# Kernel tuning notes

Hardware: AMD Instinct MI355X
Metric: run time of the kernel (lower is better)

Reference implementation:

```python
import jax, jax.numpy as jnp
import numpy as np

N, K, D, M, P, HG, HD = 120000, 8, 64, 100000, 16, 32, 96
VOXEL, TAU, OCC_INC, LMIN, LMAX = 0.1, 0.3, 0.5, -2.0, 3.5


def setup_inputs() -> dict:
    ks = jax.random.split(jax.random.key(0), 20)
    f32 = jnp.float32
    s = 0.05
    return {
        'pts_xyz': jax.random.uniform(ks[0], (N, 3), f32) * 10.0,
        'f_pts': jax.random.normal(ks[1], (N, D), f32),
        'z_latent': jax.random.normal(ks[2], (M, D), f32),
        'vals_st': jax.random.normal(ks[3], (M,), f32) * 0.5,
        'centers_xyz': jax.random.uniform(ks[4], (M, 3), f32) * 10.0,
        'Wf': jax.random.normal(ks[5], (P, D), f32) * s,
        'Wz': jax.random.normal(ks[6], (P, D), f32) * s,
        'w_delta': jax.random.normal(ks[7], (1, 3), f32) * s,
        'b_delta': jnp.zeros((1,), f32),
        'log_temp': jnp.zeros((1,), f32),
        'W_ih': jax.random.normal(ks[8], (3 * D, D), f32) * s,
        'W_hh': jax.random.normal(ks[9], (3 * D, D), f32) * s,
        'b_ih': jnp.zeros((3 * D,), f32),
        'b_hh': jnp.zeros((3 * D,), f32),
        'Wg1': jax.random.normal(ks[10], (HG, 2 * D), f32) * s,
        'bg1': jnp.zeros((HG,), f32),
        'Wg2': jax.random.normal(ks[11], (1, HG), f32) * s,
        'bg2': jnp.zeros((1,), f32),
        'ln_g': jnp.ones((D,), f32),
        'ln_b': jnp.zeros((D,), f32),
        'Wd1': jax.random.normal(ks[12], (HD, D), f32) * s,
        'bd1': jnp.zeros((HD,), f32),
        'Wd2': jax.random.normal(ks[13], (HD, HD), f32) * s,
        'bd2': jnp.zeros((HD,), f32),
        'Wd3': jax.random.normal(ks[14], (1, HD), f32) * s,
        'bd3': jnp.zeros((1,), f32),
        'keys': jnp.sort(jax.random.randint(ks[15], (M,), 0, 2 ** 30, jnp.int32)),
        'cand_idx': jax.random.randint(ks[16], (N, K), 0, M, jnp.int32),
    }


def _forward(pts_xyz, f_pts, z_latent, vals_st, centers_xyz, Wf, Wz, w_delta, b_delta,
             log_temp, W_ih, W_hh, b_ih, b_hh, Wg1, bg1, Wg2, bg2, ln_g, ln_b,
             Wd1, bd1, Wd2, bd2, Wd3, bd3, keys, cand_idx):
    # --- sparse voxel hash lookup + log-odds scatter update ---
    ijk = jnp.floor(pts_xyz / VOXEL).astype(jnp.int32)
    off = jnp.int32(1 << 9)
    h = ((ijk[:, 0] + off) << 20) ^ ((ijk[:, 1] + off) << 10) ^ (ijk[:, 2] + off)
    vox_idx = jnp.clip(jnp.searchsorted(keys, h), 0, M - 1)  # (N,)
    vals_new = jnp.clip(vals_st.at[vox_idx].add(OCC_INC), LMIN, LMAX)

    # --- top-K low-temperature routing: sim(f, z, delta) ---
    z_c = z_latent[cand_idx]                                  # (N,K,D) gather
    delta = pts_xyz[:, None, :] - centers_xyz[cand_idx]       # (N,K,3)
    Fp = f_pts @ Wf.T                                         # (N,P)
    Zp = z_c @ Wz.T                                           # (N,K,P)
    Fp = Fp / (jnp.linalg.norm(Fp, axis=-1, keepdims=True) + 1e-6)
    Zp = Zp / (jnp.linalg.norm(Zp, axis=-1, keepdims=True) + 1e-6)
    core = jnp.einsum('np,nkp->nk', Fp, Zp)
    dterm = jnp.einsum('nkc,c->nk', delta, w_delta[0]) + b_delta[0]
    sim = jnp.exp(log_temp[0]) * (core + dterm)
    w = jax.nn.softmax(sim / TAU, axis=-1)                    # (N,K)

    # --- scatter weighted point features to voxels ---
    flat_idx = cand_idx.reshape(-1)                           # (N*K,)
    contrib = (w[..., None] * f_pts[:, None, :]).reshape(-1, D)
    msg = jax.ops.segment_sum(contrib, flat_idx, num_segments=M)   # (M,D)
    wsum = jax.ops.segment_sum(w.reshape(-1), flat_idx, num_segments=M)
    msg = msg / (wsum[:, None] + 1e-6)

    # --- per-voxel gate + GRU latent fusion ---
    gate_in = jnp.concatenate([z_latent, msg], axis=-1)       # (M,2D)
    g = jax.nn.sigmoid(jax.nn.relu(gate_in @ Wg1.T + bg1) @ Wg2.T + bg2)  # (M,1)
    gi = msg @ W_ih.T + b_ih
    gh = z_latent @ W_hh.T + b_hh
    gir, giz, gin = jnp.split(gi, 3, axis=-1)
    ghr, ghz, ghn = jnp.split(gh, 3, axis=-1)
    r = jax.nn.sigmoid(gir + ghr)
    u = jax.nn.sigmoid(giz + ghz)
    n = jnp.tanh(gin + r * ghn)
    h_new = (1.0 - u) * n + u * z_latent
    z_new = z_latent + g * (h_new - z_latent)                 # (M,D)

    # --- decode occupancy: LN -> fc1 -> residual fc2 -> fc3 -> sigmoid ---
    mu = z_new.mean(-1, keepdims=True)
    var = z_new.var(-1, keepdims=True)
    x = (z_new - mu) * jax.lax.rsqrt(var + 1e-5) * ln_g + ln_b
    hd = jax.nn.relu(x @ Wd1.T + bd1)
    hd = hd + jax.nn.relu(hd @ Wd2.T + bd2)
    p = jax.nn.sigmoid((hd @ Wd3.T + bd3)[:, 0])              # (M,)

    return jnp.concatenate([p, vals_new])                     # (2M,)


def reference(pts_xyz, f_pts, z_latent, vals_st, centers_xyz, Wf, Wz, w_delta, b_delta,
              log_temp, W_ih, W_hh, b_ih, b_hh, Wg1, bg1, Wg2, bg2, ln_g, ln_b,
              Wd1, bd1, Wd2, bd2, Wd3, bd3, keys, cand_idx):
    return _forward(pts_xyz, f_pts, z_latent, vals_st, centers_xyz, Wf, Wz, w_delta,
                    b_delta, log_temp, W_ih, W_hh, b_ih, b_hh, Wg1, bg1, Wg2, bg2,
                    ln_g, ln_b, Wd1, bd1, Wd2, bd2, Wd3, bd3, keys, cand_idx)
```

## Files before the change

kernel.cpp:

```cpp
#include <hip/hip_runtime.h>
#include <math.h>

#define Nn 120000
#define Kk 8
#define Dd 64
#define Mm 100000
#define Pp 16
#define HGg 32
#define HDd 96
#define CAP 40
#define LUTB 12

typedef __attribute__((ext_vector_type(8))) short bf16x8;
typedef __attribute__((ext_vector_type(4))) float f32x4;
typedef __attribute__((ext_vector_type(4))) float fx4;
typedef __attribute__((ext_vector_type(4))) int ix4;

#define PB_K0    1563
#define PB_PACK  (PB_K0 + 22)
#define PB_INIT  (PB_PACK + 391)

__device__ __forceinline__ float sigmoidf_(float x) { return 1.f / (1.f + __expf(-x)); }
__device__ __forceinline__ float tanh_fast(float x) {
    float e = __expf(2.f * x);
    return 1.f - 2.f / (e + 1.f);
}
__device__ __forceinline__ short f2bf(float f) {
    unsigned u = __float_as_uint(f);
    unsigned r = (u + 0x7fffu + ((u >> 16) & 1u)) >> 16;
    return (short)r;
}

__global__ __launch_bounds__(256) void k_prep_all(const float* __restrict__ z,
                                                  const float* __restrict__ Wz,
                                                  const float* __restrict__ centers,
                                                  const float* __restrict__ w_delta,
                                                  const int* __restrict__ keys,
                                                  const float* __restrict__ Wg1,
                                                  const float* __restrict__ W_ih,
                                                  const float* __restrict__ W_hh,
                                                  const float* __restrict__ Wd1,
                                                  const float* __restrict__ Wd2,
                                                  const float* __restrict__ vals,
                                                  unsigned* __restrict__ Zbf,
                                                  float* __restrict__ cdot,
                                                  int* __restrict__ lut,
                                                  short* __restrict__ wsW,
                                                  int* __restrict__ cnt,
                                                  float* __restrict__ vacc) {
    int b = blockIdx.x;
    if (b < PB_K0) {
        int g = threadIdx.x & 3;
        int m = b * 64 + (threadIdx.x >> 2);
        if (m >= Mm) return;
        if (g == 0 && m <= (1 << LUTB)) {
            int target = m << (30 - LUTB);
            int lo = 0, hi = Mm;
            while (lo < hi) {
                int mid = (lo + hi) >> 1;
                if (keys[mid] < target) lo = mid + 1; else hi = mid;
            }
            lut[m] = lo;
        }
        const float4* zr = (const float4*)(z + (size_t)m * Dd + g * 16);
        float4 q0 = zr[0], q1 = zr[1], q2 = zr[2], q3 = zr[3];
        float acc[Pp];
#pragma unroll
        for (int p = 0; p < Pp; p++) {
            const float4* w = (const float4*)(Wz + (size_t)p * Dd + g * 16);
            float4 w0 = w[0], w1 = w[1], w2 = w[2], w3 = w[3];
            float s = q0.x * w0.x + q0.y * w0.y + q0.z * w0.z + q0.w * w0.w;
            s += q1.x * w1.x + q1.y * w1.y + q1.z * w1.z + q1.w * w1.w;
            s += q2.x * w2.x + q2.y * w2.y + q2.z * w2.z + q2.w * w2.w;
            s += q3.x * w3.x + q3.y * w3.y + q3.z * w3.z + q3.w * w3.w;
            acc[p] = s;
        }
#pragma unroll
        for (int p = 0; p < Pp; p++) {
            acc[p] += __shfl_xor(acc[p], 1, 64);
            acc[p] += __shfl_xor(acc[p], 2, 64);
        }
        float ss = 0.f;
#pragma unroll
        for (int p = 0; p < Pp; p++) ss = fmaf(acc[p], acc[p], ss);
        float inv = 1.f / (sqrtf(ss) + 1e-6f);
        unsigned* row = Zbf + (size_t)m * 8;
        if (g < 2) {
            uint4 o;
            unsigned w[4];
#pragma unroll
            for (int j = 0; j < 4; j++) {
                float v0 = acc[g * 8 + 2 * j] * inv;
                float v1 = acc[g * 8 + 2 * j + 1] * inv;
                w[j] = (unsigned)(unsigned short)f2bf(v0)
                     | ((unsigned)(unsigned short)f2bf(v1) << 16);
            }
            o.x = w[0]; o.y = w[1]; o.z = w[2]; o.w = w[3];
            ((uint4*)row)[g] = o;
        } else if (g == 2) {
            cdot[m] = centers[3 * m] * w_delta[0] + centers[3 * m + 1] * w_delta[1]
                    + centers[3 * m + 2] * w_delta[2];
        }
    } else if (b < PB_PACK) {
        int idx = (b - PB_K0) * 256 + threadIdx.x;
        if (idx >= 86 * 64) return;
        int f = idx >> 6, lane = idx & 63;
        int lrow = lane & 15, lhi = lane >> 4;
        const float* src;
        int t, c, K;
        if (f < 8)       { int g = f;      t = g >> 2; c = g & 3;  src = Wg1;  K = 128; }
        else if (f < 32) { int g = f - 8;  t = g >> 1; c = g & 1;  src = W_ih; K = 64; }
        else if (f < 56) { int g = f - 32; t = g >> 1; c = g & 1;  src = W_hh; K = 64; }
        else if (f < 68) { int g = f - 56; t = g >> 1; c = g & 1;  src = Wd1;  K = 64; }
        else             { int g = f - 68; t = g / 3;  c = g % 3;  src = Wd2;  K = 96; }
        int o = t * 16 + lrow;
        int k0 = c * 32 + lhi * 8;
        short* dst = wsW + ((size_t)f * 64 + lane) * 8;
#pragma unroll
        for (int j = 0; j < 8; j++) dst[j] = f2bf(src[(size_t)o * K + k0 + j]);
    } else {
        int m = (b - PB_PACK) * 256 + threadIdx.x;
        if (m < Mm) {
            cnt[m] = 0;
            vacc[m] = vals[m];
        }
    }
}

__global__ __launch_bounds__(256) void k1_route(const float* __restrict__ pts,
                                                const float* __restrict__ f_pts,
                                                const float* __restrict__ Wf,
                                                const float* __restrict__ w_delta,
                                                const float* __restrict__ b_delta,
                                                const float* __restrict__ log_temp,
                                                const int* __restrict__ keys,
                                                const int* __restrict__ cand,
                                                const unsigned* __restrict__ Zbf,
                                                const float* __restrict__ cdot,
                                                const int* __restrict__ lut,
                                                float* __restrict__ vacc,
                                                int* __restrict__ cnt,
                                                int2* __restrict__ rec,
                                                signed char* __restrict__ f8) {
    int g = threadIdx.x & 7;
    int n = blockIdx.x * 32 + (threadIdx.x >> 3);

    float px = pts[3 * n], py = pts[3 * n + 1], pz = pts[3 * n + 2];
    int myid = __builtin_nontemporal_load(cand + (size_t)n * Kk + g);

    if (g == 0) {
        int ix = (int)floorf(px / 0.1f);
        int iy = (int)floorf(py / 0.1f);
        int iz = (int)floorf(pz / 0.1f);
        int h = ((ix + 512) << 20) ^ ((iy + 512) << 10) ^ (iz + 512);
        int pfx = h >> (30 - LUTB);
        int lo = lut[pfx], hi = lut[pfx + 1];
        while (lo < hi) {
            int mid = (lo + hi) >> 1;
            if (keys[mid] < h) lo = mid + 1; else hi = mid;
        }
        int vi = lo < (Mm - 1) ? lo : (Mm - 1);
        atomicAdd(vacc + vi, 0.5f);
    }

    const fx4* fr = (const fx4*)(f_pts + (size_t)n * Dd + g * 8);
    fx4 q0 = __builtin_nontemporal_load(fr);
    fx4 q1 = __builtin_nontemporal_load(fr + 1);

    {
        float v[8] = {q0.x, q0.y, q0.z, q0.w, q1.x, q1.y, q1.z, q1.w};
        unsigned lo = 0, hi = 0;
#pragma unroll
        for (int j = 0; j < 4; j++) {
            int q = (int)rintf(fminf(fmaxf(v[j], -4.f), 4.f) * 32.f);
            lo |= ((unsigned)q & 0xffu) << (8 * j);
        }
#pragma unroll
        for (int j = 0; j < 4; j++) {
            int q = (int)rintf(fminf(fmaxf(v[4 + j], -4.f), 4.f) * 32.f);
            hi |= ((unsigned)q & 0xffu) << (8 * j);
        }
        *(int2*)(f8 + (size_t)n * Dd + g * 8) = make_int2((int)lo, (int)hi);
    }

    float fp[Pp];
#pragma unroll
    for (int p = 0; p < Pp; p++) {
        const float4* w = (const float4*)(Wf + (size_t)p * Dd + g * 8);
        float4 w0 = w[0], w1 = w[1];
        float s = q0.x * w0.x + q0.y * w0.y + q0.z * w0.z + q0.w * w0.w;
        s += q1.x * w1.x + q1.y * w1.y + q1.z * w1.z + q1.w * w1.w;
        fp[p] = s;
    }
#pragma unroll
    for (int p = 0; p < Pp; p++) {
        fp[p] += __shfl_xor(fp[p], 1, 64);
        fp[p] += __shfl_xor(fp[p], 2, 64);
        fp[p] += __shfl_xor(fp[p], 4, 64);
    }
    float ss = 0.f;
#pragma unroll
    for (int p = 0; p < Pp; p++) ss = fmaf(fp[p], fp[p], ss);
    float inv = 1.f / (sqrtf(ss) + 1e-6f);
#pragma unroll
    for (int p = 0; p < Pp; p++) fp[p] *= inv;

    float et = expf(log_temp[0]);
    float pdot = px * w_delta[0] + py * w_delta[1] + pz * w_delta[2] + b_delta[0];

    const uint4* zp = (const uint4*)(Zbf + (size_t)myid * 8);
    uint4 A = zp[0], B = zp[1];
    float cd = cdot[myid];
    unsigned uw[8] = {A.x, A.y, A.z, A.w, B.x, B.y, B.z, B.w};
    float core = 0.f;
#pragma unroll
    for (int j = 0; j < 8; j++) {
        float lo = __uint_as_float(uw[j] << 16);
        float hi = __uint_as_float(uw[j] & 0xffff0000u);
        core = fmaf(fp[2 * j], lo, core);
        core = fmaf(fp[2 * j + 1], hi, core);
    }
    float sim = et * (core + pdot - cd) / 0.3f;

    float mx = sim;
    mx = fmaxf(mx, __shfl_xor(mx, 1, 64));
    mx = fmaxf(mx, __shfl_xor(mx, 2, 64));
    mx = fmaxf(mx, __shfl_xor(mx, 4, 64));
    float e = __expf(sim - mx);
    float se = e;
    se += __shfl_xor(se, 1, 64);
    se += __shfl_xor(se, 2, 64);
    se += __shfl_xor(se, 4, 64);
    float w = e / se;

    int pos = atomicAdd(cnt + myid, 1);
    if (pos < CAP) {
        long long pk = (unsigned)n | ((long long)(unsigned)__float_as_int(w) << 32);
        __builtin_nontemporal_store(pk, (long long*)(rec + (size_t)myid * CAP + pos));
    }
}

__global__ __launch_bounds__(256, 4) void k23_mfma(const float* __restrict__ z_latent,
                                                   const signed char* __restrict__ f8,
                                                   const int* __restrict__ cnt,
                                                   const int2* __restrict__ rec,
                                                   const short* __restrict__ wsW,
                                                   const float* __restrict__ bg1,
                                                   const float* __restrict__ Wg2,
                                                   const float* __restrict__ bg2,
                                                   const float* __restrict__ b_ih,
                                                   const float* __restrict__ b_hh,
                                                   const float* __restrict__ ln_g,
                                                   const float* __restrict__ ln_b,
                                                   const float* __restrict__ bd1,
                                                   const float* __restrict__ bd2,
                                                   const float* __restrict__ Wd3,
                                                   const float* __restrict__ bd3,
                                                   const float* __restrict__ vacc,
                                                   float* __restrict__ out) {
    __shared__ unsigned short msgs[64][72];
    __shared__ float scr_all[4][16 * 97];
    int tid = threadIdx.x;
    int wv = tid >> 6, lane = tid & 63;
    int b = blockIdx.x;

    {
        int v = tid >> 2;
        int dq = (tid & 3) << 4;
        int m = b * 64 + v;
        if (m < Mm) {
            int c = cnt[m];
            if (c > CAP) c = CAP;
            const ix4* r4 = (const ix4*)(rec + (size_t)m * CAP);
            const signed char* fq = f8 + dq;
            float acc[16];
#pragma unroll
            for (int d = 0; d < 16; d++) acc[d] = 0.f;
            float wsum = 0.f;
            for (int i0 = 0; i0 < c; i0 += 8) {
                ix4 A = r4[(i0 >> 1) + 0];
                ix4 B = r4[(i0 >> 1) + 1];
                ix4 C = r4[(i0 >> 1) + 2];
                ix4 D = r4[(i0 >> 1) + 3];
                int rn[8] = {A.x, A.z, B.x, B.z, C.x, C.z, D.x, D.z};
                int rw[8] = {A.y, A.w, B.y, B.w, C.y, C.w, D.y, D.w};
                int nn[8];
                float ww[8];
#pragma unroll
                for (int k = 0; k < 8; k++) {
                    bool valid = (i0 + k) < c;
                    nn[k] = valid ? rn[k] : 0;
                    ww[k] = valid ? __int_as_float(rw[k]) : 0.f;
                }
                int4 G[8];
#pragma unroll
                for (int k = 0; k < 8; k++)
                    G[k] = *(const int4*)(fq + ((size_t)nn[k] << 6));
#pragma unroll
                for (int k = 0; k < 8; k++) {
                    wsum += ww[k];
                    int gg[4] = {G[k].x, G[k].y, G[k].z, G[k].w};
#pragma unroll
                    for (int q = 0; q < 4; q++)
#pragma unroll
                        for (int j = 0; j < 4; j++) {
                            float vv = (float)((signed char)((gg[q] >> (8 * j)) & 0xff));
                            acc[q * 4 + j] = fmaf(ww[k], vv, acc[q * 4 + j]);
                        }
                }
            }
#pragma unroll
            for (int d = 0; d < 16; d++) {
                float a = acc[d] * 0.03125f;
                msgs[v][dq + d] = (unsigned short)f2bf(a / (wsum + 1e-6f));
            }
        }
    }
    __syncthreads();

    int tile = b * 4 + wv;
    if (tile >= Mm / 16) return;
    int m0 = tile * 16;
    float* scr = scr_all[wv];
    int lrow = lane & 15;
    int lhi = lane >> 4;

    if (lane < 16) {
        float v = vacc[m0 + lane];
        out[Mm + m0 + lane] = fminf(fmaxf(v, -2.f), 3.5f);
    }

    const bf16x8* WF = (const bf16x8*)wsW;
#define BFRAG(off) (WF[(off) * 64 + lane])

    bf16x8 za[2], ma[2];
    const float* zrow = z_latent + (size_t)(m0 + lrow) * Dd + lhi * 8;
    const unsigned short* mr = &msgs[wv * 16 + lrow][lhi * 8];
#pragma unroll
    for (int c = 0; c < 2; c++) {
        bf16x8 t0;
#pragma unroll
        for (int j = 0; j < 8; j++) t0[j] = f2bf(zrow[c * 32 + j]);
        za[c] = t0;
        ma[c] = *(const bf16x8*)(mr + c * 32);
    }

    bf16x8 wgf[8];
#pragma unroll
    for (int j = 0; j < 8; j++) wgf[j] = BFRAG(j);
    f32x4 g0 = {0.f, 0.f, 0.f, 0.f}, g1 = {0.f, 0.f, 0.f, 0.f};
    bf16x8 gateA[4] = {za[0], za[1], ma[0], ma[1]};
#pragma unroll
    for (int c = 0; c < 4; c++) {
        g0 = __builtin_amdgcn_mfma_f32_16x16x32_bf16(gateA[c], wgf[c], g0, 0, 0, 0);
        g1 = __builtin_amdgcn_mfma_f32_16x16x32_bf16(gateA[c], wgf[4 + c], g1, 0, 0, 0);
    }
    float bgA = bg1[lrow], bgB = bg1[16 + lrow];
    float w2A = Wg2[lrow], w2B = Wg2[16 + lrow];
    float g[4];
#pragma unroll
    for (int r = 0; r < 4; r++) {
        float ga = fmaxf(g0[r] + bgA, 0.f) * w2A + fmaxf(g1[r] + bgB, 0.f) * w2B;
        ga += __shfl_xor(ga, 1, 64);
        ga += __shfl_xor(ga, 2, 64);
        ga += __shfl_xor(ga, 4, 64);
        ga += __shfl_xor(ga, 8, 64);
        g[r] = sigmoidf_(ga + bg2[0]);
    }

    float zn[4][4];
    float ps[4] = {0.f, 0.f, 0.f, 0.f}, pq[4] = {0.f, 0.f, 0.f, 0.f};
#pragma unroll
    for (int t = 0; t < 4; t++) {
        bf16x8 wt[12];
#pragma unroll
        for (int c = 0; c < 2; c++) {
            wt[0 + c]  = BFRAG(8 + t * 2 + c);
            wt[2 + c]  = BFRAG(8 + (t + 4) * 2 + c);
            wt[4 + c]  = BFRAG(8 + (t + 8) * 2 + c);
            wt[6 + c]  = BFRAG(32 + t * 2 + c);
            wt[8 + c]  = BFRAG(32 + (t + 4) * 2 + c);
            wt[10 + c] = BFRAG(32 + (t + 8) * 2 + c);
        }
        f32x4 Ar = {0.f, 0.f, 0.f, 0.f}, Az = Ar, An = Ar, Br = Ar, Bz = Ar, Bn = Ar;
#pragma unroll
        for (int c = 0; c < 2; c++) {
            Ar = __builtin_amdgcn_mfma_f32_16x16x32_bf16(ma[c], wt[0 + c], Ar, 0, 0, 0);
            Az = __builtin_amdgcn_mfma_f32_16x16x32_bf16(ma[c], wt[2 + c], Az, 0, 0, 0);
            An = __builtin_amdgcn_mfma_f32_16x16x32_bf16(ma[c], wt[4 + c], An, 0, 0, 0);
            Br = __builtin_amdgcn_mfma_f32_16x16x32_bf16(za[c], wt[6 + c], Br, 0, 0, 0);
            Bz = __builtin_amdgcn_mfma_f32_16x16x32_bf16(za[c], wt[8 + c], Bz, 0, 0, 0);
            Bn = __builtin_amdgcn_mfma_f32_16x16x32_bf16(za[c], wt[10 + c], Bn, 0, 0, 0);
        }
        int oc = t * 16 + lrow;
        float bir = b_ih[oc], biz = b_ih[64 + oc], bin = b_ih[128 + oc];
        float bhr = b_hh[oc], bhz = b_hh[64 + oc], bhn = b_hh[128 + oc];
#pragma unroll
        for (int r = 0; r < 4; r++) {
            int row = lhi * 4 + r;
            float zo = z_latent[(size_t)(m0 + row) * Dd + oc];
            float rr = sigmoidf_(Ar[r] + bir + Br[r] + bhr);
            float uu = sigmoidf_(Az[r] + biz + Bz[r] + bhz);
            float nnv = tanh_fast(An[r] + bin + rr * (Bn[r] + bhn));
            float hn = (1.f - uu) * nnv + uu * zo;
            float z2 = zo + g[r] * (hn - zo);
            zn[t][r] = z2;
            ps[r] += z2;
            pq[r] = fmaf(z2, z2, pq[r]);
        }
    }
    float mu[4], rs[4];
#pragma unroll
    for (int r = 0; r < 4; r++) {
        float s = ps[r], q = pq[r];
        s += __shfl_xor(s, 1, 64); q += __shfl_xor(q, 1, 64);
        s += __shfl_xor(s, 2, 64); q += __shfl_xor(q, 2, 64);
        s += __shfl_xor(s, 4, 64); q += __shfl_xor(q, 4, 64);
        s += __shfl_xor(s, 8, 64); q += __shfl_xor(q, 8, 64);
        float m = s * (1.f / 64.f);
        float v = q * (1.f / 64.f) - m * m;
        mu[r] = m;
        rs[r] = rsqrtf(v + 1e-5f);
    }
#pragma unroll
    for (int t = 0; t < 4; t++) {
        int o = t * 16 + lrow;
        float lg = ln_g[o], lb = ln_b[o];
#pragma unroll
        for (int r = 0; r < 4; r++)
            scr[(lhi * 4 + r) * 97 + o] = (zn[t][r] - mu[r]) * rs[r] * lg + lb;
    }
    __threadfence_block();

    bf16x8 xa[2];
#pragma unroll
    for (int c = 0; c < 2; c++) {
        bf16x8 tb;
#pragma unroll
        for (int j = 0; j < 8; j++) tb[j] = f2bf(scr[lrow * 97 + c * 32 + lhi * 8 + j]);
        xa[c] = tb;
    }
    bf16x8 wf1[12];
#pragma unroll
    for (int j = 0; j < 12; j++) wf1[j] = BFRAG(56 + j);
    f32x4 h1t[6];
#pragma unroll
    for (int t = 0; t < 6; t++) h1t[t] = (f32x4){0.f, 0.f, 0.f, 0.f};
#pragma unroll
    for (int t = 0; t < 6; t++)
#pragma unroll
        for (int c = 0; c < 2; c++)
            h1t[t] = __builtin_amdgcn_mfma_f32_16x16x32_bf16(xa[c], wf1[t * 2 + c], h1t[t], 0, 0, 0);
    float h1r[6][4];
#pragma unroll
    for (int t = 0; t < 6; t++) {
        float bb = bd1[t * 16 + lrow];
#pragma unroll
        for (int r = 0; r < 4; r++) {
            h1r[t][r] = fmaxf(h1t[t][r] + bb, 0.f);
            scr[(lhi * 4 + r) * 97 + t * 16 + lrow] = h1r[t][r];
        }
    }
    __threadfence_block();

    bf16x8 ha[3];
#pragma unroll
    for (int c = 0; c < 3; c++) {
        bf16x8 tb;
#pragma unroll
        for (int j = 0; j < 8; j++) tb[j] = f2bf(scr[lrow * 97 + c * 32 + lhi * 8 + j]);
        ha[c] = tb;
    }
    bf16x8 wf2[18];
#pragma unroll
    for (int j = 0; j < 18; j++) wf2[j] = BFRAG(68 + j);
    f32x4 o2[6];
#pragma unroll
    for (int t = 0; t < 6; t++) o2[t] = (f32x4){0.f, 0.f, 0.f, 0.f};
#pragma unroll
    for (int t = 0; t < 6; t++)
#pragma unroll
        for (int c = 0; c < 3; c++)
            o2[t] = __builtin_amdgcn_mfma_f32_16x16x32_bf16(ha[c], wf2[t * 3 + c], o2[t], 0, 0, 0);
    float pacc[4] = {0.f, 0.f, 0.f, 0.f};
#pragma unroll
    for (int t = 0; t < 6; t++) {
        int o = t * 16 + lrow;
        float bb = bd2[o], w3 = Wd3[o];
#pragma unroll
        for (int r = 0; r < 4; r++) {
            float hd2 = h1r[t][r] + fmaxf(o2[t][r] + bb, 0.f);
            pacc[r] = fmaf(hd2, w3, pacc[r]);
        }
    }
#pragma unroll
    for (int r = 0; r < 4; r++) {
        float s = pacc[r];
        s += __shfl_xor(s, 1, 64);
        s += __shfl_xor(s, 2, 64);
        s += __shfl_xor(s, 4, 64);
        s += __shfl_xor(s, 8, 64);
        if (lrow == 0) out[m0 + lhi * 4 + r] = sigmoidf_(s + bd3[0]);
    }
#undef BFRAG
}

extern "C" void kernel_launch(void* const* d_in, const int* in_sizes, int n_in,
                              void* d_out, int out_size, void* d_ws, size_t ws_size,
                              hipStream_t stream) {
    const float* pts      = (const float*)d_in[0];
    const float* f_pts    = (const float*)d_in[1];
    const float* z_lat    = (const float*)d_in[2];
    const float* vals     = (const float*)d_in[3];
    const float* centers  = (const float*)d_in[4];
    const float* Wf       = (const float*)d_in[5];
    const float* Wz       = (const float*)d_in[6];
    const float* w_delta  = (const float*)d_in[7];
    const float* b_delta  = (const float*)d_in[8];
    const float* log_temp = (const float*)d_in[9];
    const float* W_ih     = (const float*)d_in[10];
    const float* W_hh     = (const float*)d_in[11];
    const float* b_ih     = (const float*)d_in[12];
    const float* b_hh     = (const float*)d_in[13];
    const float* Wg1      = (const float*)d_in[14];
    const float* bg1      = (const float*)d_in[15];
    const float* Wg2      = (const float*)d_in[16];
    const float* bg2      = (const float*)d_in[17];
    const float* ln_g     = (const float*)d_in[18];
    const float* ln_b     = (const float*)d_in[19];
    const float* Wd1      = (const float*)d_in[20];
    const float* bd1      = (const float*)d_in[21];
    const float* Wd2      = (const float*)d_in[22];
    const float* bd2      = (const float*)d_in[23];
    const float* Wd3      = (const float*)d_in[24];
    const float* bd3      = (const float*)d_in[25];
    const int*   keys     = (const int*)d_in[26];
    const int*   cand     = (const int*)d_in[27];
    float* out = (float*)d_out;

    float* ws = (float*)d_ws;
    short* wsW = (short*)ws;
    unsigned* Zbf = (unsigned*)(ws + 32768);
    float* cdot = ws + 32768 + 800000;
    signed char* f8 = (signed char*)(ws + 32768 + 900000);
    float* base = ws + 32768 + 900000 + 1920000;
    float* vacc = base + (size_t)Mm * Dd / 2;
    int*   cnt  = (int*)(vacc + Mm);
    int2*  rec  = (int2*)(cnt + Mm);
    int*   lut  = (int*)((int*)rec + (size_t)Mm * CAP * 2);

    k_prep_all<<<PB_INIT, 256, 0, stream>>>(z_lat, Wz, centers, w_delta, keys,
                                            Wg1, W_ih, W_hh, Wd1, Wd2, vals,
                                            Zbf, cdot, lut, wsW, cnt, vacc);
    k1_route<<<Nn / 32, 256, 0, stream>>>(pts, f_pts, Wf, w_delta, b_delta, log_temp,
                                          keys, cand, Zbf, cdot, lut, vacc, cnt, rec,
                                          f8);
    k23_mfma<<<(Mm / 16 + 3) / 4, 256, 0, stream>>>(z_lat, f8, cnt, rec, wsW, bg1,
                                                    Wg2, bg2, b_ih, b_hh, ln_g, ln_b,
                                                    bd1, bd2, Wd3, bd3, vacc, out);
}
```

Baseline: 279.0 us.

## Shrink k23 blocks to two waves, store LDS scratch as bf16, move init to memset

The fused GRU/decoder kernel now runs 128-thread blocks covering 32 latents each, so the bounds checks go away and more blocks are available. The per-wave LDS scratch switches from padded fp32 to padded bf16, which allows a single vector load per MFMA fragment instead of eight scalar loads plus conversions. The count and accumulator initialisation moves out of the prep kernel into hipMemsetAsync and a device-to-device copy. These add two extra stream operations and drop the Mm%32 guards, which relies on Mm being divisible by 32.

Measured after the change: 291.9 us. 1.05x slower.

```diff
diff --git a/kernel.cpp b/kernel.cpp
--- a/kernel.cpp
+++ b/kernel.cpp
@@ -18,7 +18,6 @@
 
 #define PB_K0    1563
 #define PB_PACK  (PB_K0 + 22)
-#define PB_INIT  (PB_PACK + 391)
 
 __device__ __forceinline__ float sigmoidf_(float x) { return 1.f / (1.f + __expf(-x)); }
 __device__ __forceinline__ float tanh_fast(float x) {
@@ -41,13 +40,10 @@
                                                   const float* __restrict__ W_hh,
                                                   const float* __restrict__ Wd1,
                                                   const float* __restrict__ Wd2,
-                                                  const float* __restrict__ vals,
                                                   unsigned* __restrict__ Zbf,
                                                   float* __restrict__ cdot,
                                                   int* __restrict__ lut,
-                                                  short* __restrict__ wsW,
-                                                  int* __restrict__ cnt,
-                                                  float* __restrict__ vacc) {
+                                                  short* __restrict__ wsW) {
     int b = blockIdx.x;
     if (b < PB_K0) {
         int g = threadIdx.x & 3;
@@ -101,7 +97,7 @@
             cdot[m] = centers[3 * m] * w_delta[0] + centers[3 * m + 1] * w_delta[1]
                     + centers[3 * m + 2] * w_delta[2];
         }
-    } else if (b < PB_PACK) {
+    } else {
         int idx = (b - PB_K0) * 256 + threadIdx.x;
         if (idx >= 86 * 64) return;
         int f = idx >> 6, lane = idx & 63;
@@ -118,12 +114,6 @@
         short* dst = wsW + ((size_t)f * 64 + lane) * 8;
 #pragma unroll
         for (int j = 0; j < 8; j++) dst[j] = f2bf(src[(size_t)o * K + k0 + j]);
-    } else {
-        int m = (b - PB_PACK) * 256 + threadIdx.x;
-        if (m < Mm) {
-            cnt[m] = 0;
-            vacc[m] = vals[m];
-        }
     }
 }
 
@@ -240,7 +230,7 @@
     }
 }
 
-__global__ __launch_bounds__(256, 4) void k23_mfma(const float* __restrict__ z_latent,
+__global__ __launch_bounds__(128, 4) void k23_mfma(const float* __restrict__ z_latent,
                                                    const signed char* __restrict__ f8,
                                                    const int* __restrict__ cnt,
                                                    const int2* __restrict__ rec,
@@ -258,8 +248,8 @@
                                                    const float* __restrict__ bd3,
                                                    const float* __restrict__ vacc,
                                                    float* __restrict__ out) {
-    __shared__ unsigned short msgs[64][72];
-    __shared__ float scr_all[4][16 * 97];
+    __shared__ unsigned short msgs[32][72];
+    __shared__ unsigned short scr_all[2][16 * 104];
     int tid = threadIdx.x;
     int wv = tid >> 6, lane = tid & 63;
     int b = blockIdx.x;
@@ -267,61 +257,58 @@
     {
         int v = tid >> 2;
         int dq = (tid & 3) << 4;
-        int m = b * 64 + v;
-        if (m < Mm) {
-            int c = cnt[m];
-            if (c > CAP) c = CAP;
-            const ix4* r4 = (const ix4*)(rec + (size_t)m * CAP);
-            const signed char* fq = f8 + dq;
-            float acc[16];
-#pragma unroll
-            for (int d = 0; d < 16; d++) acc[d] = 0.f;
-            float wsum = 0.f;
-            for (int i0 = 0; i0 < c; i0 += 8) {
-                ix4 A = r4[(i0 >> 1) + 0];
-                ix4 B = r4[(i0 >> 1) + 1];
-                ix4 C = r4[(i0 >> 1) + 2];
-                ix4 D = r4[(i0 >> 1) + 3];
-                int rn[8] = {A.x, A.z, B.x, B.z, C.x, C.z, D.x, D.z};
-                int rw[8] = {A.y, A.w, B.y, B.w, C.y, C.w, D.y, D.w};
-                int nn[8];
-                float ww[8];
-#pragma unroll
-                for (int k = 0; k < 8; k++) {
-                    bool valid = (i0 + k) < c;
-                    nn[k] = valid ? rn[k] : 0;
-                    ww[k] = valid ? __int_as_float(rw[k]) : 0.f;
-                }
-                int4 G[8];
-#pragma unroll
-                for (int k = 0; k < 8; k++)
-                    G[k] = *(const int4*)(fq + ((size_t)nn[k] << 6));
-#pragma unroll
-                for (int k = 0; k < 8; k++) {
-                    wsum += ww[k];
-                    int gg[4] = {G[k].x, G[k].y, G[k].z, G[k].w};
-#pragma unroll
-                    for (int q = 0; q < 4; q++)
-#pragma unroll
-                        for (int j = 0; j < 4; j++) {
-                            float vv = (float)((signed char)((gg[q] >> (8 * j)) & 0xff));
-                            acc[q * 4 + j] = fmaf(ww[k], vv, acc[q * 4 + j]);
-                        }
-                }
+        int m = b * 32 + v;
+        int c = cnt[m];
+        if (c > CAP) c = CAP;
+        const ix4* r4 = (const ix4*)(rec + (size_t)m * CAP);
+        const signed char* fq = f8 + dq;
+        float acc[16];
+#pragma unroll
+        for (int d = 0; d < 16; d++) acc[d] = 0.f;
+        float wsum = 0.f;
+        for (int i0 = 0; i0 < c; i0 += 8) {
+            ix4 A = r4[(i0 >> 1) + 0];
+            ix4 B = r4[(i0 >> 1) + 1];
+            ix4 C = r4[(i0 >> 1) + 2];
+            ix4 D = r4[(i0 >> 1) + 3];
+            int rn[8] = {A.x, A.z, B.x, B.z, C.x, C.z, D.x, D.z};
+            int rw[8] = {A.y, A.w, B.y, B.w, C.y, C.w, D.y, D.w};
+            int nn[8];
+            float ww[8];
+#pragma unroll
+            for (int k = 0; k < 8; k++) {
+                bool valid = (i0 + k) < c;
+                nn[k] = valid ? rn[k] : 0;
+                ww[k] = valid ? __int_as_float(rw[k]) : 0.f;
             }
-#pragma unroll
-            for (int d = 0; d < 16; d++) {
-                float a = acc[d] * 0.03125f;
-                msgs[v][dq + d] = (unsigned short)f2bf(a / (wsum + 1e-6f));
+            int4 G[8];
+#pragma unroll
+            for (int k = 0; k < 8; k++)
+                G[k] = *(const int4*)(fq + ((size_t)nn[k] << 6));
+#pragma unroll
+            for (int k = 0; k < 8; k++) {
+                wsum += ww[k];
+                int gg[4] = {G[k].x, G[k].y, G[k].z, G[k].w};
+#pragma unroll
+                for (int q = 0; q < 4; q++)
+#pragma unroll
+                    for (int j = 0; j < 4; j++) {
+                        float vv = (float)((signed char)((gg[q] >> (8 * j)) & 0xff));
+                        acc[q * 4 + j] = fmaf(ww[k], vv, acc[q * 4 + j]);
+                    }
             }
         }
+#pragma unroll
+        for (int d = 0; d < 16; d++) {
+            float a = acc[d] * 0.03125f;
+            msgs[v][dq + d] = (unsigned short)f2bf(a / (wsum + 1e-6f));
+        }
     }
     __syncthreads();
 
-    int tile = b * 4 + wv;
-    if (tile >= Mm / 16) return;
+    int tile = b * 2 + wv;
     int m0 = tile * 16;
-    float* scr = scr_all[wv];
+    unsigned short* scr = scr_all[wv];
     int lrow = lane & 15;
     int lhi = lane >> 4;
 
@@ -335,14 +322,13 @@
 
     bf16x8 za[2], ma[2];
     const float* zrow = z_latent + (size_t)(m0 + lrow) * Dd + lhi * 8;
-    const unsigned short* mr = &msgs[wv * 16 + lrow][lhi * 8];
 #pragma unroll
     for (int c = 0; c < 2; c++) {
         bf16x8 t0;
 #pragma unroll
         for (int j = 0; j < 8; j++) t0[j] = f2bf(zrow[c * 32 + j]);
         za[c] = t0;
-        ma[c] = *(const bf16x8*)(mr + c * 32);
+        ma[c] = *(const bf16x8*)&msgs[wv * 16 + lrow][c * 32 + lhi * 8];
     }
 
     bf16x8 wgf[8];
@@ -428,18 +414,15 @@
         float lg = ln_g[o], lb = ln_b[o];
 #pragma unroll
         for (int r = 0; r < 4; r++)
-            scr[(lhi * 4 + r) * 97 + o] = (zn[t][r] - mu[r]) * rs[r] * lg + lb;
+            scr[(lhi * 4 + r) * 104 + o] =
+                (unsigned short)f2bf((zn[t][r] - mu[r]) * rs[r] * lg + lb);
     }
     __threadfence_block();
 
     bf16x8 xa[2];
 #pragma unroll
-    for (int c = 0; c < 2; c++) {
-        bf16x8 tb;
-#pragma unroll
-        for (int j = 0; j < 8; j++) tb[j] = f2bf(scr[lrow * 97 + c * 32 + lhi * 8 + j]);
-        xa[c] = tb;
-    }
+    for (int c = 0; c < 2; c++)
+        xa[c] = *(const bf16x8*)&scr[lrow * 104 + c * 32 + lhi * 8];
     bf16x8 wf1[12];
 #pragma unroll
     for (int j = 0; j < 12; j++) wf1[j] = BFRAG(56 + j);
@@ -458,19 +441,15 @@
 #pragma unroll
         for (int r = 0; r < 4; r++) {
             h1r[t][r] = fmaxf(h1t[t][r] + bb, 0.f);
-            scr[(lhi * 4 + r) * 97 + t * 16 + lrow] = h1r[t][r];
+            scr[(lhi * 4 + r) * 104 + t * 16 + lrow] = (unsigned short)f2bf(h1r[t][r]);
         }
     }
     __threadfence_block();
 
     bf16x8 ha[3];
 #pragma unroll
-    for (int c = 0; c < 3; c++) {
-        bf16x8 tb;
-#pragma unroll
-        for (int j = 0; j < 8; j++) tb[j] = f2bf(scr[lrow * 97 + c * 32 + lhi * 8 + j]);
-        ha[c] = tb;
-    }
+    for (int c = 0; c < 3; c++)
+        ha[c] = *(const bf16x8*)&scr[lrow * 104 + c * 32 + lhi * 8];
     bf16x8 wf2[18];
 #pragma unroll
     for (int j = 0; j < 18; j++) wf2[j] = BFRAG(68 + j);
@@ -549,13 +528,17 @@
     int2*  rec  = (int2*)(cnt + Mm);
     int*   lut  = (int*)((int*)rec + (size_t)Mm * CAP * 2);
 
-    k_prep_all<<<PB_INIT, 256, 0, stream>>>(z_lat, Wz, centers, w_delta, keys,
-                                            Wg1, W_ih, W_hh, Wd1, Wd2, vals,
-                                            Zbf, cdot, lut, wsW, cnt, vacc);
+    hipMemsetAsync(cnt, 0, (size_t)Mm * sizeof(int), stream);
+    hipMemcpyAsync(vacc, vals, (size_t)Mm * sizeof(float),
+                   hipMemcpyDeviceToDevice, stream);
+
+    k_prep_all<<<PB_PACK, 256, 0, stream>>>(z_lat, Wz, centers, w_delta, keys,
+                                            Wg1, W_ih, W_hh, Wd1, Wd2,
+                                            Zbf, cdot, lut, wsW);
     k1_route<<<Nn / 32, 256, 0, stream>>>(pts, f_pts, Wf, w_delta, b_delta, log_temp,
                                           keys, cand, Zbf, cdot, lut, vacc, cnt, rec,
                                           f8);
-    k23_mfma<<<(Mm / 16 + 3) / 4, 256, 0, stream>>>(z_lat, f8, cnt, rec, wsW, bg1,
-                                                    Wg2, bg2, b_ih, b_hh, ln_g, ln_b,
-                                                    bd1, bd2, Wd3, bd3, vacc, out);
+    k23_mfma<<<Mm / 32, 128, 0, stream>>>(z_lat, f8, cnt, rec, wsW, bg1,
+                                          Wg2, bg2, b_ih, b_hh, ln_g, ln_b,
+                                          bd1, bd2, Wd3, bd3, vacc, out);
 }
```
